# Kernel optimization log

Measured on AMD Instinct MI355X. Metric: run time of the kernel, lower is better.

Reference implementation:

```python
import jax, jax.numpy as jnp
import numpy as np

B, S, HID = 2, 2048, 2048
H, KV, D = 32, 4, 128
G = H // KV
EPS = 1e-6
SCALE = D ** -0.5
ROPE_THETA = 1000000.0


def setup_inputs() -> dict:
    key = jax.random.key(0)
    ks = jax.random.split(key, 6)
    hidden_states = jax.random.normal(ks[0], (B, S, HID), jnp.float32)
    # real RoPE tables (position_embeddings passed into forward)
    inv_freq = 1.0 / (ROPE_THETA ** (np.arange(0, D, 2, dtype=np.float32) / D))
    ang = np.arange(S, dtype=np.float32)[:, None] * inv_freq[None, :]  # [S, D/2]
    emb = np.concatenate([ang, ang], axis=-1)  # [S, D]
    cos = jnp.broadcast_to(jnp.asarray(np.cos(emb)), (B, S, D))
    sin = jnp.broadcast_to(jnp.asarray(np.sin(emb)), (B, S, D))
    sd = 0.02
    wq = jax.random.normal(ks[1], (H * D, HID), jnp.float32) * sd
    wk = jax.random.normal(ks[2], (KV * D, HID), jnp.float32) * sd
    wv = jax.random.normal(ks[3], (KV * D, HID), jnp.float32) * sd
    wo = jax.random.normal(ks[4], (HID, H * D), jnp.float32) * sd
    q_norm_w = jnp.ones((D,), jnp.float32)
    k_norm_w = jnp.ones((D,), jnp.float32)
    return {"hidden_states": hidden_states, "cos": cos, "sin": sin,
            "wq": wq, "wk": wk, "wv": wv, "wo": wo,
            "q_norm_w": q_norm_w, "k_norm_w": k_norm_w}


def _rms_norm(x, w):
    var = jnp.mean(jnp.square(x), axis=-1, keepdims=True)
    return x * jax.lax.rsqrt(var + EPS) * w


def _rotate_half(x):
    x1, x2 = jnp.split(x, 2, axis=-1)
    return jnp.concatenate([-x2, x1], axis=-1)


def _rope(x, cos, sin):
    # x: [B,S,N,D]; cos/sin: [B,S,1,D] (unsqueeze_dim=2)
    return x * cos + _rotate_half(x) * sin


def reference(hidden_states, cos, sin, wq, wk, wv, wo, q_norm_w, k_norm_w):
    x = hidden_states
    q = jnp.einsum('bsh,oh->bso', x, wq).reshape(B, S, H, D)
    k = jnp.einsum('bsh,oh->bso', x, wk).reshape(B, S, KV, D)
    v = jnp.einsum('bsh,oh->bso', x, wv).reshape(B, S, KV, D)
    q = _rms_norm(q, q_norm_w)
    k = _rms_norm(k, k_norm_w)
    c = cos[:, :, None, :]
    s = sin[:, :, None, :]
    q = _rope(q, c, s)
    k = _rope(k, c, s)
    # GQA causal attention, BSND layout
    qg = q.reshape(B, S, KV, G, D)
    scores = jnp.einsum('bqkgd,bskd->bkgqs', qg, k) * SCALE  # [B,KV,G,Sq,Sk]
    causal = jnp.tril(jnp.ones((S, S), bool))
    scores = jnp.where(causal, scores, jnp.finfo(scores.dtype).min)
    p = jax.nn.softmax(scores, axis=-1)
    out = jnp.einsum('bkgqs,bskd->bqkgd', p, v).reshape(B, S, H * D)
    return jnp.einsum('bso,ho->bsh', out, wo)
```

## Files before the change

### kernel.cpp

```cpp
#include <hip/hip_runtime.h>
#include <hip/hip_bf16.h>

typedef __attribute__((ext_vector_type(8))) short short8;
typedef __attribute__((ext_vector_type(4))) float f32x4;

#define DEVI static __device__ __forceinline__

constexpr int Bb = 2, Ss = 2048, Hh = 32, KVc = 4, Dc = 128;
constexpr float EPSc = 1e-6f;
constexpr float SCALEc = 0.08838834764831845f;

DEVI float bf2f(short s) {
  unsigned u = ((unsigned)(unsigned short)s) << 16;
  float f; __builtin_memcpy(&f, &u, 4); return f;
}
DEVI short f2bf(float f) {
  __hip_bfloat16 h = __float2bfloat16(f);
  unsigned short u; __builtin_memcpy(&u, &h, 2); return (short)u;
}

#define GLDS(gsrc, ldst) __builtin_amdgcn_global_load_lds( \
    (const __attribute__((address_space(1))) void*)(gsrc), \
    (__attribute__((address_space(3))) void*)(ldst), 16, 0, 0)

__global__ void cvt_kernel(const float* __restrict__ in, short* __restrict__ out, int n4) {
  int i = blockIdx.x * blockDim.x + threadIdx.x;
  if (i < n4) {
    float4 v = ((const float4*)in)[i];
    short4 o;
    o.x = f2bf(v.x); o.y = f2bf(v.y); o.z = f2bf(v.z); o.w = f2bf(v.w);
    ((short4*)out)[i] = o;
  }
}

template<int MODE>
__launch_bounds__(256, 2)
__global__ void gemm_bt(const short* __restrict__ A,
                        const short* __restrict__ B0,
                        const short* __restrict__ B1,
                        const short* __restrict__ B2,
                        short* __restrict__ oq,
                        short* __restrict__ ok,
                        short* __restrict__ ov,
                        float* __restrict__ of,
                        int K)
{
  __shared__ short lA[128 * 32];
  __shared__ short lB[128 * 32];
  const int tid = threadIdx.x;
  const int lane = tid & 63;
  const int wvi = tid >> 6;
  const int l15 = lane & 15, g = lane >> 4;
  const int m0 = blockIdx.x * 128;
  const int nt = blockIdx.y;
  const short* Bp; int n0, region;
  if (MODE == 0) {
    if (nt < 32)      { Bp = B0; n0 = nt * 128;        region = 0; }
    else if (nt < 36) { Bp = B1; n0 = (nt - 32) * 128; region = 1; }
    else              { Bp = B2; n0 = (nt - 36) * 128; region = 2; }
  } else { Bp = B0; n0 = nt * 128; region = 3; }

  const int wm = (wvi >> 1) * 64, wn = (wvi & 1) * 64;
  const int srow = tid >> 2, schunk = tid & 3;

  f32x4 acc[4][4] = {};

  for (int k0 = 0; k0 < K; k0 += 32) {
    __syncthreads();
#pragma unroll
    for (int c = 0; c < 2; ++c) {
      int row = c * 64 + srow;
      int gc = schunk ^ ((row >> 1) & 3);
      GLDS(A  + (size_t)(m0 + row) * K + k0 + gc * 8, lA + (c * 256 + tid) * 8);
      GLDS(Bp + (size_t)(n0 + row) * K + k0 + gc * 8, lB + (c * 256 + tid) * 8);
    }
    __syncthreads();
    short8 afr[4], bfr[4];
#pragma unroll
    for (int i = 0; i < 4; ++i) {
      int ra = wm + i * 16 + l15;
      afr[i] = *(const short8*)(lA + ra * 32 + ((g ^ ((ra >> 1) & 3)) * 8));
      int rb = wn + i * 16 + l15;
      bfr[i] = *(const short8*)(lB + rb * 32 + ((g ^ ((rb >> 1) & 3)) * 8));
    }
#pragma unroll
    for (int mi = 0; mi < 4; ++mi)
#pragma unroll
      for (int ni = 0; ni < 4; ++ni)
        acc[mi][ni] = __builtin_amdgcn_mfma_f32_16x16x32_bf16(afr[mi], bfr[ni], acc[mi][ni], 0, 0, 0);
  }

#pragma unroll
  for (int mi = 0; mi < 4; ++mi)
#pragma unroll
    for (int ni = 0; ni < 4; ++ni)
#pragma unroll
      for (int r = 0; r < 4; ++r) {
        int m = m0 + wm + mi * 16 + g * 4 + r;
        int n = n0 + wn + ni * 16 + l15;
        float v = acc[mi][ni][r];
        if (MODE == 1) {
          of[(size_t)m * 2048 + n] = v;
        } else if (region == 0) {
          oq[(size_t)m * 4096 + n] = f2bf(v);
        } else {
          int b = m >> 11, s = m & 2047, kvi = n >> 7, d = n & 127;
          if (region == 1)
            ok[(((size_t)b * KVc + kvi) * Ss + s) * 128 + d] = f2bf(v);
          else
            ov[(((size_t)b * KVc + kvi) * 128 + d) * Ss + s] = f2bf(v);
        }
      }
}

template<bool ISQ>
__global__ void rmsnorm_rope(short* __restrict__ buf, const float* __restrict__ w,
                             const float* __restrict__ cosb, const float* __restrict__ sinb)
{
  const int lane = threadIdx.x & 63;
  const int wvi = threadIdx.x >> 6;
  const int i = blockIdx.x * 4 + wvi;
  short* row;
  int b, s;
  if (ISQ) {
    int m = i >> 5, h = i & 31;
    b = m >> 11; s = m & 2047;
    row = buf + (size_t)m * 4096 + h * 128;
  } else {
    s = i & 2047; int bkv = i >> 11; b = bkv >> 2;
    row = buf + (size_t)i * 128;
  }
  float x1 = bf2f(row[lane]), x2 = bf2f(row[lane + 64]);
  float ss = x1 * x1 + x2 * x2;
#pragma unroll
  for (int o = 32; o; o >>= 1) ss += __shfl_xor(ss, o);
  float inv = rsqrtf(ss * (1.0f / 128.0f) + EPSc);
  const float* cp = cosb + ((size_t)b * Ss + s) * Dc;
  const float* sp = sinb + ((size_t)b * Ss + s) * Dc;
  float n1 = x1 * inv * w[lane], n2 = x2 * inv * w[lane + 64];
  row[lane]      = f2bf(n1 * cp[lane]      - n2 * sp[lane]);
  row[lane + 64] = f2bf(n2 * cp[lane + 64] + n1 * sp[lane + 64]);
}

__launch_bounds__(256, 2)
__global__ void attn_fwd(const short* __restrict__ qb,
                         const short* __restrict__ kbuf,
                         const short* __restrict__ vtbuf,
                         short* __restrict__ ob)
{
  __shared__ short lK[2][64 * 128];
  __shared__ short lV[2][128 * 64];
  __shared__ short lP[4][32 * 32];
  const int tid = threadIdx.x, lane = tid & 63, wvi = tid >> 6;
  const int l15 = lane & 15, g = lane >> 4;
  const int pi = blockIdx.x, h = blockIdx.y, b = blockIdx.z;
  const int kv = h >> 3;
  const short* kp = kbuf  + ((size_t)b * KVc + kv) * Ss * 128;
  const short* vp = vtbuf + ((size_t)b * KVc + kv) * 128 * Ss;
  const int krow = tid >> 4, kch = tid & 15;
  const int vrow = tid >> 3, vch = tid & 7;

  for (int which = 0; which < 2; ++which) {
    const int qt = which ? (15 - pi) : pi;
    const int qwb = qt * 128 + wvi * 32;
    const int nkt = 2 * qt + 2;

    short8 qf[2][4];
#pragma unroll
    for (int qs = 0; qs < 2; ++qs)
#pragma unroll
      for (int dc = 0; dc < 4; ++dc)
        qf[qs][dc] = *(const short8*)(qb + (size_t)(b * Ss + qwb + qs * 16 + l15) * 4096
                                         + h * 128 + dc * 32 + g * 8);

    f32x4 oacc[2][8] = {};
    float mrun[2] = { -__builtin_inff(), -__builtin_inff() };
    float lrun[2] = { 0.f, 0.f };

    auto STAGE = [&](int kt, int bufi) {
      const int kb0 = kt * 64;
#pragma unroll
      for (int c = 0; c < 4; ++c) {
        int r = c * 16 + krow;
        int gc = kch ^ (r & 7);
        GLDS(kp + (size_t)(kb0 + r) * 128 + gc * 8, &lK[bufi][(c * 256 + tid) * 8]);
      }
#pragma unroll
      for (int c = 0; c < 4; ++c) {
        int r = c * 32 + vrow;
        int gc = vch ^ (r & 7);
        GLDS(vp + (size_t)r * Ss + kb0 + gc * 8, &lV[bufi][(c * 256 + tid) * 8]);
      }
    };

    STAGE(0, 0);
    STAGE(1, 1);

    for (int kt = 0; kt < nkt; ++kt) {
      const int cb = kt & 1;
      if (kt + 1 < nkt) asm volatile("s_waitcnt vmcnt(8)" ::: "memory");
      else              asm volatile("s_waitcnt vmcnt(0)" ::: "memory");
      __builtin_amdgcn_s_barrier();
      asm volatile("" ::: "memory");

#pragma unroll
      for (int half = 0; half < 2; ++half) {
        const int kb0 = kt * 64 + half * 32;
        if (kb0 <= qwb + 31) {
          short8 kf[2][4];
#pragma unroll
          for (int ks = 0; ks < 2; ++ks)
#pragma unroll
            for (int dc = 0; dc < 4; ++dc) {
              int row = half * 32 + ks * 16 + l15;
              kf[ks][dc] = *(const short8*)(&lK[cb][0] + row * 128 + (((dc * 4 + g) ^ (row & 7)) * 8));
            }
          f32x4 st[2][2] = {};
#pragma unroll
          for (int qs = 0; qs < 2; ++qs)
#pragma unroll
            for (int ks = 0; ks < 2; ++ks)
#pragma unroll
              for (int dc = 0; dc < 4; ++dc)
                st[qs][ks] = __builtin_amdgcn_mfma_f32_16x16x32_bf16(kf[ks][dc], qf[qs][dc], st[qs][ks], 0, 0, 0);

          const bool need_mask = (kb0 + 31 > qwb);
#pragma unroll
          for (int qs = 0; qs < 2; ++qs) {
            const int qg = qwb + qs * 16 + l15;
            float p[8];
            float tmax = -__builtin_inff();
#pragma unroll
            for (int ks = 0; ks < 2; ++ks)
#pragma unroll
              for (int r = 0; r < 4; ++r) {
                float v = st[qs][ks][r] * SCALEc;
                if (need_mask && (kb0 + ks * 16 + g * 4 + r > qg)) v = -__builtin_inff();
                p[ks * 4 + r] = v;
                tmax = fmaxf(tmax, v);
              }
            tmax = fmaxf(tmax, __shfl_xor(tmax, 16));
            tmax = fmaxf(tmax, __shfl_xor(tmax, 32));
            float mnew = fmaxf(mrun[qs], tmax);
            float scl = __expf(mrun[qs] - mnew);
            float rsum = 0.f;
#pragma unroll
            for (int j = 0; j < 8; ++j) { p[j] = __expf(p[j] - mnew); rsum += p[j]; }
            rsum += __shfl_xor(rsum, 16);
            rsum += __shfl_xor(rsum, 32);
            lrun[qs] = lrun[qs] * scl + rsum;
            mrun[qs] = mnew;
            {
              int row = qs * 16 + l15;
              int sw = (row >> 1) & 3;
              short* pr = lP[wvi] + row * 32;
#pragma unroll
              for (int ks = 0; ks < 2; ++ks) {
                int idx = (((2 * ks + (g >> 1)) ^ sw) * 8) + (g & 1) * 4;
                short4 pw;
                pw.x = f2bf(p[ks * 4 + 0]);
                pw.y = f2bf(p[ks * 4 + 1]);
                pw.z = f2bf(p[ks * 4 + 2]);
                pw.w = f2bf(p[ks * 4 + 3]);
                *(short4*)(pr + idx) = pw;
              }
            }
#pragma unroll
            for (int r = 0; r < 4; ++r) {
              float sc = __shfl(scl, g * 4 + r);
#pragma unroll
              for (int dt = 0; dt < 8; ++dt)
                oacc[qs][dt][r] *= sc;
            }
          }
          asm volatile("" ::: "memory");
          short8 vf[8];
#pragma unroll
          for (int dt = 0; dt < 8; ++dt) {
            int row = dt * 16 + l15;
            vf[dt] = *(const short8*)(&lV[cb][0] + row * 64 + (((half * 4 + g) ^ (row & 7)) * 8));
          }
#pragma unroll
          for (int qs = 0; qs < 2; ++qs) {
            int row = qs * 16 + l15;
            short8 pf = *(const short8*)(lP[wvi] + row * 32 + ((g ^ ((row >> 1) & 3)) * 8));
#pragma unroll
            for (int dt = 0; dt < 8; ++dt)
              oacc[qs][dt] = __builtin_amdgcn_mfma_f32_16x16x32_bf16(pf, vf[dt], oacc[qs][dt], 0, 0, 0);
          }
          asm volatile("" ::: "memory");
        }
      }

      asm volatile("" ::: "memory");
      __builtin_amdgcn_s_barrier();
      if (kt + 2 < nkt) STAGE(kt + 2, cb);
    }

#pragma unroll
    for (int qs = 0; qs < 2; ++qs)
#pragma unroll
      for (int r = 0; r < 4; ++r) {
        float inv = 1.0f / __shfl(lrun[qs], g * 4 + r);
        int qrow = qwb + qs * 16 + g * 4 + r;
        short* op = ob + (size_t)(b * Ss + qrow) * 4096 + h * 128;
#pragma unroll
        for (int dt = 0; dt < 8; ++dt)
          op[dt * 16 + l15] = f2bf(oacc[qs][dt][r] * inv);
      }
  }
}

extern "C" void kernel_launch(void* const* d_in, const int* in_sizes, int n_in,
                              void* d_out, int out_size, void* d_ws, size_t ws_size,
                              hipStream_t stream) {
  const float* x    = (const float*)d_in[0];
  const float* cosb = (const float*)d_in[1];
  const float* sinb = (const float*)d_in[2];
  const float* wq   = (const float*)d_in[3];
  const float* wk   = (const float*)d_in[4];
  const float* wv   = (const float*)d_in[5];
  const float* wo   = (const float*)d_in[6];
  const float* qw   = (const float*)d_in[7];
  const float* kw   = (const float*)d_in[8];

  size_t off = 0;
  auto alloc = [&](size_t bytes) {
    char* p = (char*)d_ws + off;
    off += (bytes + 255) & ~(size_t)255;
    return p;
  };
  short* x_bf  = (short*)alloc((size_t)8388608 * 2);
  short* wq_bf = (short*)alloc((size_t)8388608 * 2);
  short* wk_bf = (short*)alloc((size_t)1048576 * 2);
  short* wv_bf = (short*)alloc((size_t)1048576 * 2);
  short* wo_bf = (short*)alloc((size_t)8388608 * 2);
  short* q_bf  = (short*)alloc((size_t)16777216 * 2);
  short* k_bf  = (short*)alloc((size_t)2097152 * 2);
  short* v_bf  = (short*)alloc((size_t)2097152 * 2);
  short* ao_bf = (short*)alloc((size_t)16777216 * 2);

  auto cv = [&](const float* s, short* d, int n) {
    int n4 = n / 4;
    cvt_kernel<<<(n4 + 255) / 256, 256, 0, stream>>>(s, d, n4);
  };
  cv(x,  x_bf,  8388608);
  cv(wq, wq_bf, 8388608);
  cv(wk, wk_bf, 1048576);
  cv(wv, wv_bf, 1048576);
  cv(wo, wo_bf, 8388608);

  gemm_bt<0><<<dim3(32, 40), 256, 0, stream>>>(x_bf, wq_bf, wk_bf, wv_bf,
                                               q_bf, k_bf, v_bf, nullptr, 2048);
  rmsnorm_rope<true><<<32768, 256, 0, stream>>>(q_bf, qw, cosb, sinb);
  rmsnorm_rope<false><<<4096, 256, 0, stream>>>(k_bf, kw, cosb, sinb);
  attn_fwd<<<dim3(8, 32, 2), 256, 0, stream>>>(q_bf, k_bf, v_bf, ao_bf);
  gemm_bt<1><<<dim3(32, 16), 256, 0, stream>>>(ao_bf, wo_bf, nullptr, nullptr,
                                               nullptr, nullptr, nullptr, (float*)d_out, 4096);
}
```

Before: 380.8 us.

## Remap GEMM blocks per XCD, fold softmax scale into Q, lazy rescale, MFMA priority

The GEMM launches become 1D, and block ids are remapped so each XCD works on a contiguous set of N tiles, which should improve L2 reuse of the weight tiles. The softmax scale is folded into Q during the RMSNorm/RoPE pass, so the per-score multiply is gone. The online softmax now rescales the running max and accumulator only when some lane's new max exceeds the old one by more than 8, skipping most rescale work; this risks larger intermediate exponent values. s_setprio brackets are added around the MFMA sections to favour matrix issue across waves.

New measurement: 385.2 us. About the same (+1.2%).

```diff
diff --git a/kernel.cpp b/kernel.cpp
--- a/kernel.cpp
+++ b/kernel.cpp
@@ -51,8 +51,10 @@
   const int lane = tid & 63;
   const int wvi = tid >> 6;
   const int l15 = lane & 15, g = lane >> 4;
-  const int m0 = blockIdx.x * 128;
-  const int nt = blockIdx.y;
+  const int bid = blockIdx.x;
+  const int xcd = bid & 7, idx = bid >> 3;
+  const int nt = (MODE == 0) ? (xcd * 5 + (idx >> 5)) : (xcd * 2 + (idx >> 5));
+  const int m0 = (idx & 31) * 128;
   const short* Bp; int n0, region;
   if (MODE == 0) {
     if (nt < 32)      { Bp = B0; n0 = nt * 128;        region = 0; }
@@ -138,8 +140,11 @@
   const float* cp = cosb + ((size_t)b * Ss + s) * Dc;
   const float* sp = sinb + ((size_t)b * Ss + s) * Dc;
   float n1 = x1 * inv * w[lane], n2 = x2 * inv * w[lane + 64];
-  row[lane]      = f2bf(n1 * cp[lane]      - n2 * sp[lane]);
-  row[lane + 64] = f2bf(n2 * cp[lane + 64] + n1 * sp[lane + 64]);
+  float o1 = n1 * cp[lane]      - n2 * sp[lane];
+  float o2 = n2 * cp[lane + 64] + n1 * sp[lane + 64];
+  if (ISQ) { o1 *= SCALEc; o2 *= SCALEc; }
+  row[lane]      = f2bf(o1);
+  row[lane + 64] = f2bf(o2);
 }
 
 __launch_bounds__(256, 2)
@@ -216,6 +221,7 @@
               kf[ks][dc] = *(const short8*)(&lK[cb][0] + row * 128 + (((dc * 4 + g) ^ (row & 7)) * 8));
             }
           f32x4 st[2][2] = {};
+          __builtin_amdgcn_s_setprio(1);
 #pragma unroll
           for (int qs = 0; qs < 2; ++qs)
 #pragma unroll
@@ -223,6 +229,7 @@
 #pragma unroll
               for (int dc = 0; dc < 4; ++dc)
                 st[qs][ks] = __builtin_amdgcn_mfma_f32_16x16x32_bf16(kf[ks][dc], qf[qs][dc], st[qs][ks], 0, 0, 0);
+          __builtin_amdgcn_s_setprio(0);
 
           const bool need_mask = (kb0 + 31 > qwb);
 #pragma unroll
@@ -234,22 +241,34 @@
             for (int ks = 0; ks < 2; ++ks)
 #pragma unroll
               for (int r = 0; r < 4; ++r) {
-                float v = st[qs][ks][r] * SCALEc;
+                float v = st[qs][ks][r];
                 if (need_mask && (kb0 + ks * 16 + g * 4 + r > qg)) v = -__builtin_inff();
                 p[ks * 4 + r] = v;
                 tmax = fmaxf(tmax, v);
               }
             tmax = fmaxf(tmax, __shfl_xor(tmax, 16));
             tmax = fmaxf(tmax, __shfl_xor(tmax, 32));
-            float mnew = fmaxf(mrun[qs], tmax);
-            float scl = __expf(mrun[qs] - mnew);
+            float m_use = mrun[qs];
+            if (__any(tmax > m_use + 8.0f)) {
+              float mnew = fmaxf(m_use, tmax);
+              float scl = __expf(m_use - mnew);
+              lrun[qs] *= scl;
+              mrun[qs] = mnew;
+#pragma unroll
+              for (int r = 0; r < 4; ++r) {
+                float sc = __shfl(scl, g * 4 + r);
+#pragma unroll
+                for (int dt = 0; dt < 8; ++dt)
+                  oacc[qs][dt][r] *= sc;
+              }
+              m_use = mnew;
+            }
             float rsum = 0.f;
 #pragma unroll
-            for (int j = 0; j < 8; ++j) { p[j] = __expf(p[j] - mnew); rsum += p[j]; }
+            for (int j = 0; j < 8; ++j) { p[j] = __expf(p[j] - m_use); rsum += p[j]; }
             rsum += __shfl_xor(rsum, 16);
             rsum += __shfl_xor(rsum, 32);
-            lrun[qs] = lrun[qs] * scl + rsum;
-            mrun[qs] = mnew;
+            lrun[qs] += rsum;
             {
               int row = qs * 16 + l15;
               int sw = (row >> 1) & 3;
@@ -265,13 +284,6 @@
                 *(short4*)(pr + idx) = pw;
               }
             }
-#pragma unroll
-            for (int r = 0; r < 4; ++r) {
-              float sc = __shfl(scl, g * 4 + r);
-#pragma unroll
-              for (int dt = 0; dt < 8; ++dt)
-                oacc[qs][dt][r] *= sc;
-            }
           }
           asm volatile("" ::: "memory");
           short8 vf[8];
@@ -280,6 +292,7 @@
             int row = dt * 16 + l15;
             vf[dt] = *(const short8*)(&lV[cb][0] + row * 64 + (((half * 4 + g) ^ (row & 7)) * 8));
           }
+          __builtin_amdgcn_s_setprio(1);
 #pragma unroll
           for (int qs = 0; qs < 2; ++qs) {
             int row = qs * 16 + l15;
@@ -288,6 +301,7 @@
             for (int dt = 0; dt < 8; ++dt)
               oacc[qs][dt] = __builtin_amdgcn_mfma_f32_16x16x32_bf16(pf, vf[dt], oacc[qs][dt], 0, 0, 0);
           }
+          __builtin_amdgcn_s_setprio(0);
           asm volatile("" ::: "memory");
         }
       }
@@ -350,11 +364,11 @@
   cv(wv, wv_bf, 1048576);
   cv(wo, wo_bf, 8388608);
 
-  gemm_bt<0><<<dim3(32, 40), 256, 0, stream>>>(x_bf, wq_bf, wk_bf, wv_bf,
-                                               q_bf, k_bf, v_bf, nullptr, 2048);
+  gemm_bt<0><<<1280, 256, 0, stream>>>(x_bf, wq_bf, wk_bf, wv_bf,
+                                       q_bf, k_bf, v_bf, nullptr, 2048);
   rmsnorm_rope<true><<<32768, 256, 0, stream>>>(q_bf, qw, cosb, sinb);
   rmsnorm_rope<false><<<4096, 256, 0, stream>>>(k_bf, kw, cosb, sinb);
   attn_fwd<<<dim3(8, 32, 2), 256, 0, stream>>>(q_bf, k_bf, v_bf, ao_bf);
-  gemm_bt<1><<<dim3(32, 16), 256, 0, stream>>>(ao_bf, wo_bf, nullptr, nullptr,
-                                               nullptr, nullptr, nullptr, (float*)d_out, 4096);
-}
+  gemm_bt<1><<<512, 256, 0, stream>>>(ao_bf, wo_bf, nullptr, nullptr,
+                                      nullptr, nullptr, nullptr, (float*)d_out, 4096);
+}
```
